# Performance work log

Measured on AMD Instinct MI355X. Metric: run time of the kernel, lower is better.

Reference implementation:

```python
import jax, jax.numpy as jnp
import numpy as np

HEADS = 8
DIM_HEAD = 64          # dim // 8
INNER = HEADS * DIM_HEAD
LANDMARKS = 256        # dim // 2
PINV_ITERS = 6
KER = 33               # residual_conv_kernel
DIM = 512


def layer_norm(x, gamma, beta, eps=1e-5):
    mu = x.mean(-1, keepdims=True)
    var = x.var(-1, keepdims=True)
    return (x - mu) / jnp.sqrt(var + eps) * gamma + beta


def moore_penrose_pinv(x, iters):
    # x: [b, h, m, m]; Newton-Schulz iteration, init z = x^T / (max colsum * max rowsum)
    abs_x = jnp.abs(x)
    col = abs_x.sum(-1)
    row = abs_x.sum(-2)
    z = jnp.swapaxes(x, -1, -2) / (jnp.max(col) * jnp.max(row))
    I = jnp.eye(x.shape[-1], dtype=x.dtype)
    for _ in range(iters):
        xz = x @ z
        z = 0.25 * z @ (13.0 * I - xz @ (15.0 * I - xz @ (7.0 * I - xz)))
    return z


def nystrom_attention(x, w_qkv, w_out, b_out, conv_w):
    b, n, _ = x.shape
    qkv = x @ w_qkv                                   # [b, n, 3*inner]
    q, k, v = jnp.split(qkv, 3, axis=-1)
    split = lambda t: t.reshape(b, n, HEADS, DIM_HEAD).transpose(0, 2, 1, 3)  # [b,h,n,dh]
    q, k, v = split(q), split(k), split(v)
    q = q * (DIM_HEAD ** -0.5)

    l = n // LANDMARKS  # n chosen divisible by num_landmarks (no padding branch)
    q_land = q.reshape(b, HEADS, LANDMARKS, l, DIM_HEAD).mean(3)  # [b,h,m,dh]
    k_land = k.reshape(b, HEADS, LANDMARKS, l, DIM_HEAD).mean(3)

    sim1 = jnp.einsum('bhid,bhjd->bhij', q, k_land)       # [b,h,n,m]
    sim2 = jnp.einsum('bhid,bhjd->bhij', q_land, k_land)  # [b,h,m,m]
    sim3 = jnp.einsum('bhid,bhjd->bhij', q_land, k)       # [b,h,m,n]
    attn1 = jax.nn.softmax(sim1, -1)
    attn2 = jax.nn.softmax(sim2, -1)
    attn3 = jax.nn.softmax(sim3, -1)

    attn2_inv = moore_penrose_pinv(attn2, PINV_ITERS)
    out = (attn1 @ attn2_inv) @ (attn3 @ v)               # [b,h,n,dh]

    # depthwise residual conv over sequence dim: Conv2d(h, h, (33,1), groups=h, no bias)
    res = jax.lax.conv_general_dilated(
        v, conv_w, window_strides=(1, 1),
        padding=((KER // 2, KER // 2), (0, 0)),
        dimension_numbers=('NCHW', 'OIHW', 'NCHW'),
        feature_group_count=HEADS)
    out = out + res

    out = out.transpose(0, 2, 1, 3).reshape(b, n, INNER)
    return out @ w_out + b_out  # dropout is identity at eval


def setup_inputs() -> dict:
    key = jax.random.key(0)
    ks = jax.random.split(key, 7)
    b, n = 4, 8192
    return {
        'x': jax.random.normal(ks[0], (b, n, DIM), dtype=jnp.float32),
        'gamma': jnp.ones((DIM,), jnp.float32),
        'beta': jnp.zeros((DIM,), jnp.float32),
        'w_qkv': jax.random.normal(ks[1], (DIM, 3 * INNER), jnp.float32) * 0.02,
        'w_out': jax.random.normal(ks[2], (INNER, DIM), jnp.float32) * 0.02,
        'b_out': jnp.zeros((DIM,), jnp.float32),
        'conv_w': jax.random.normal(ks[3], (HEADS, 1, KER, 1), jnp.float32) * 0.02,
    }


def reference(x, gamma, beta, w_qkv, w_out, b_out, conv_w):
    return x + nystrom_attention(layer_norm(x, gamma, beta), w_qkv, w_out, b_out, conv_w)
```

## Files before the change

### kernel.cpp

```cpp
#include <hip/hip_runtime.h>
#include <hip/hip_bf16.h>
#include <utility>


typedef unsigned short ushort_t;
typedef __attribute__((ext_vector_type(8))) short short8;
typedef __attribute__((ext_vector_type(4))) float f32x4;
typedef __attribute__((ext_vector_type(16))) float f32x16;

#define GPTR(p) ((const __attribute__((address_space(1))) void*)(p))
#define LPTR(p) ((__attribute__((address_space(3))) void*)(p))

__device__ inline float bf2f(ushort_t u) {
  union { unsigned int i; float f; } x; x.i = ((unsigned int)u) << 16; return x.f;
}
__device__ inline ushort_t f2bf(float f) {
  union { float f; unsigned int i; } x; x.f = f;
  unsigned int r = x.i + 0x7FFF + ((x.i >> 16) & 1);
  return (ushort_t)(r >> 16);
}

__global__ __launch_bounds__(256) void ln_bf16(const float* __restrict__ x,
                                               const float* __restrict__ g,
                                               const float* __restrict__ be,
                                               ushort_t* __restrict__ out) {
  int row = blockIdx.x; int t = threadIdx.x;
  const float* xr = x + (size_t)row * 512;
  float2 v = *(const float2*)(xr + 2 * t);
  float s = v.x + v.y, qs = v.x * v.x + v.y * v.y;
#pragma unroll
  for (int o = 32; o > 0; o >>= 1) { s += __shfl_xor(s, o); qs += __shfl_xor(qs, o); }
  __shared__ float ps[4], pq[4];
  if ((t & 63) == 0) { ps[t >> 6] = s; pq[t >> 6] = qs; }
  __syncthreads();
  s = ps[0] + ps[1] + ps[2] + ps[3];
  qs = pq[0] + pq[1] + pq[2] + pq[3];
  float mu = s * (1.f / 512.f);
  float var = qs * (1.f / 512.f) - mu * mu;
  float rstd = rsqrtf(var + 1e-5f);
  float o0 = (v.x - mu) * rstd * g[2 * t] + be[2 * t];
  float o1 = (v.y - mu) * rstd * g[2 * t + 1] + be[2 * t + 1];
  unsigned int pk = (unsigned int)f2bf(o0) | ((unsigned int)f2bf(o1) << 16);
  *(unsigned int*)(out + (size_t)row * 512 + 2 * t) = pk;
}

__global__ __launch_bounds__(256) void wtrans(const float* __restrict__ in,
                                              ushort_t* __restrict__ outw,
                                              int K, int N) {
  __shared__ float tile[64][65];
  int kb = blockIdx.x * 64, nb = blockIdx.y * 64, t = threadIdx.x;
  for (int i = t; i < 4096; i += 256) {
    int r = i >> 6, c = i & 63;
    tile[r][c] = in[(size_t)(kb + r) * N + nb + c];
  }
  __syncthreads();
  for (int i = t; i < 4096; i += 256) {
    int r = i >> 6, c = i & 63;
    outw[(size_t)(nb + r) * K + kb + c] = f2bf(tile[c][r]);
  }
}

__global__ __launch_bounds__(256) void gemm_qkv_mfma(const short* __restrict__ Abf,
                                                     const short* __restrict__ Wt,
                                                     ushort_t* __restrict__ q,
                                                     ushort_t* __restrict__ k,
                                                     ushort_t* __restrict__ vT) {
  int bm0 = blockIdx.x * 128, bn0 = blockIdx.y * 128;
  __shared__ __align__(16) short As[128 * 32];
  __shared__ __align__(16) short Bs[128 * 32];
  int t = threadIdx.x, l = t & 63, w = t >> 6;
  int wr = w >> 1, wc = w & 1;
  int arow = w * 32 + (l >> 2);
  int akoff = (l & 3) * 8;
  const short* ag = Abf + (size_t)(bm0 + arow) * 512 + akoff;
  const short* bg = Wt + (size_t)(bn0 + arow) * 512 + akoff;
  short* Adst = As + w * 1024;
  short* Bdst = Bs + w * 1024;
  int lr = l & 15, lk = (l >> 4) * 8;
  const short* Ard = As + (wr * 64 + lr) * 32 + lk;
  const short* Brd = Bs + (wc * 64 + lr) * 32 + lk;
  f32x4 acc[16];
#pragma unroll
  for (int i = 0; i < 16; i++) acc[i] = (f32x4){0.f, 0.f, 0.f, 0.f};
  for (int k0 = 0; k0 < 512; k0 += 32) {
    __builtin_amdgcn_global_load_lds(GPTR(ag + k0), LPTR(Adst), 16, 0, 0);
    __builtin_amdgcn_global_load_lds(GPTR(ag + k0 + 16 * 512), LPTR(Adst + 512), 16, 0, 0);
    __builtin_amdgcn_global_load_lds(GPTR(bg + k0), LPTR(Bdst), 16, 0, 0);
    __builtin_amdgcn_global_load_lds(GPTR(bg + k0 + 16 * 512), LPTR(Bdst + 512), 16, 0, 0);
    __syncthreads();
    short8 af[4], bf[4];
#pragma unroll
    for (int mf = 0; mf < 4; mf++) af[mf] = *(const short8*)(Ard + mf * 512);
#pragma unroll
    for (int nf = 0; nf < 4; nf++) bf[nf] = *(const short8*)(Brd + nf * 512);
#pragma unroll
    for (int mf = 0; mf < 4; mf++)
#pragma unroll
      for (int nf = 0; nf < 4; nf++)
        acc[mf * 4 + nf] = __builtin_amdgcn_mfma_f32_16x16x32_bf16(af[mf], bf[nf], acc[mf * 4 + nf], 0, 0, 0);
    __syncthreads();
  }
#pragma unroll
  for (int mf = 0; mf < 4; mf++)
#pragma unroll
    for (int nf = 0; nf < 4; nf++) {
      int gn = bn0 + wc * 64 + nf * 16 + (l & 15);
      int part = gn >> 9, head = (gn >> 6) & 7, d = gn & 63;
      int rbase = bm0 + wr * 64 + mf * 16 + ((l >> 4) << 2);
      int bhead = (rbase >> 13) * 8 + head;
      if (part == 2) {
        union { ushort_t s[4]; unsigned long long u; } p4;
#pragma unroll
        for (int i = 0; i < 4; i++) p4.s[i] = f2bf(acc[mf * 4 + nf][i]);
        *(unsigned long long*)(vT + ((size_t)bhead * 64 + d) * 8192 + (rbase & 8191)) = p4.u;
      } else {
#pragma unroll
        for (int i = 0; i < 4; i++) {
          int gm = rbase + i;
          size_t dst = ((size_t)bhead * 8192 + (gm & 8191)) * 64 + d;
          float val = acc[mf * 4 + nf][i];
          if (part == 0) q[dst] = f2bf(val * 0.125f);
          else k[dst] = f2bf(val);
        }
      }
    }
}

__global__ __launch_bounds__(256) void gemm_out_mfma(const ushort_t* __restrict__ outh,
                                                     const short* __restrict__ Wt,
                                                     const float* __restrict__ x,
                                                     const float* __restrict__ bo,
                                                     float* __restrict__ out) {
  int bn0 = blockIdx.x * 128, bm0 = blockIdx.y * 128;
  __shared__ __align__(16) short As[128 * 32];
  __shared__ __align__(16) short Bs[128 * 32];
  int t = threadIdx.x, l = t & 63, w = t >> 6;
  int wr = w >> 1, wc = w & 1;
  int arow = w * 32 + (l >> 2);
  int akoff = (l & 3) * 8;
  int gm0 = bm0 + arow, gm1 = gm0 + 16;
  const short* bg = Wt + (size_t)(bn0 + arow) * 512 + akoff;
  short* Adst = As + w * 1024;
  short* Bdst = Bs + w * 1024;
  int lr = l & 15, lk = (l >> 4) * 8;
  const short* Ard = As + (wr * 64 + lr) * 32 + lk;
  const short* Brd = Bs + (wc * 64 + lr) * 32 + lk;
  f32x4 acc[16];
#pragma unroll
  for (int i = 0; i < 16; i++) acc[i] = (f32x4){0.f, 0.f, 0.f, 0.f};
  for (int k0 = 0; k0 < 512; k0 += 32) {
    int kk = k0 + akoff;
    const ushort_t* a0 = outh + ((size_t)((gm0 >> 13) * 8 + (kk >> 6)) * 8192 + (gm0 & 8191)) * 64 + (kk & 63);
    const ushort_t* a1 = outh + ((size_t)((gm1 >> 13) * 8 + (kk >> 6)) * 8192 + (gm1 & 8191)) * 64 + (kk & 63);
    __builtin_amdgcn_global_load_lds(GPTR(a0), LPTR(Adst), 16, 0, 0);
    __builtin_amdgcn_global_load_lds(GPTR(a1), LPTR(Adst + 512), 16, 0, 0);
    __builtin_amdgcn_global_load_lds(GPTR(bg + k0), LPTR(Bdst), 16, 0, 0);
    __builtin_amdgcn_global_load_lds(GPTR(bg + k0 + 16 * 512), LPTR(Bdst + 512), 16, 0, 0);
    __syncthreads();
    short8 af[4], bf[4];
#pragma unroll
    for (int mf = 0; mf < 4; mf++) af[mf] = *(const short8*)(Ard + mf * 512);
#pragma unroll
    for (int nf = 0; nf < 4; nf++) bf[nf] = *(const short8*)(Brd + nf * 512);
#pragma unroll
    for (int mf = 0; mf < 4; mf++)
#pragma unroll
      for (int nf = 0; nf < 4; nf++)
        acc[mf * 4 + nf] = __builtin_amdgcn_mfma_f32_16x16x32_bf16(af[mf], bf[nf], acc[mf * 4 + nf], 0, 0, 0);
    __syncthreads();
  }
#pragma unroll
  for (int mf = 0; mf < 4; mf++)
#pragma unroll
    for (int nf = 0; nf < 4; nf++) {
      int gn = bn0 + wc * 64 + nf * 16 + (l & 15);
      int rbase = bm0 + wr * 64 + mf * 16 + ((l >> 4) << 2);
#pragma unroll
      for (int i = 0; i < 4; i++) {
        int gm = rbase + i;
        size_t o = (size_t)gm * 512 + gn;
        out[o] = x[o] + bo[gn] + acc[mf * 4 + nf][i];
      }
    }
}

__global__ void land_kernel(const ushort_t* __restrict__ q, const ushort_t* __restrict__ k,
                            float* __restrict__ qlf, float* __restrict__ klf,
                            ushort_t* __restrict__ qlh, ushort_t* __restrict__ klh) {
  int bh = blockIdx.y, mi = blockIdx.x, d = threadIdx.x;
  size_t base = ((size_t)bh * 8192 + (size_t)mi * 32) * 64 + d;
  float sq = 0.f, sk = 0.f;
  for (int j = 0; j < 32; j++) {
    sq += bf2f(q[base + (size_t)j * 64]);
    sk += bf2f(k[base + (size_t)j * 64]);
  }
  size_t o = ((size_t)bh * 256 + mi) * 64 + d;
  float aq = sq * (1.f / 32.f), ak = sk * (1.f / 32.f);
  qlf[o] = aq; klf[o] = ak;
  qlh[o] = f2bf(aq); klh[o] = f2bf(ak);
}

__global__ __launch_bounds__(256) void sim2_kernel(const float* __restrict__ ql,
                                                   const float* __restrict__ kl,
                                                   ushort_t* __restrict__ xh,
                                                   ushort_t* __restrict__ xl) {
  int bh = blockIdx.y, row = blockIdx.x, t = threadIdx.x;
  __shared__ float qrow[64];
  __shared__ float red[256];
  if (t < 64) qrow[t] = ql[((size_t)bh * 256 + row) * 64 + t];
  __syncthreads();
  const float* kr = kl + ((size_t)bh * 256 + t) * 64;
  float s = 0.f;
#pragma unroll
  for (int kd = 0; kd < 64; kd++) s = fmaf(qrow[kd], kr[kd], s);
  red[t] = s; __syncthreads();
  for (int off = 128; off > 0; off >>= 1) { if (t < off) red[t] = fmaxf(red[t], red[t + off]); __syncthreads(); }
  float mx = red[0]; __syncthreads();
  float pv = __expf(s - mx);
  red[t] = pv; __syncthreads();
  for (int off = 128; off > 0; off >>= 1) { if (t < off) red[t] += red[t + off]; __syncthreads(); }
  float pn = pv / red[0];
  size_t idx = ((size_t)bh << 16) + (size_t)row * 256 + t;
  ushort_t hi = f2bf(pn);
  xh[idx] = hi;
  xl[idx] = f2bf(pn - bf2f(hi));
}

__global__ __launch_bounds__(256) void abssum_kernel(const ushort_t* __restrict__ xh,
                                                     const ushort_t* __restrict__ xl,
                                                     float* __restrict__ rowsum,
                                                     float* __restrict__ colsum) {
  int bh = blockIdx.x, t = threadIdx.x;
  size_t off = (size_t)bh << 16;
  float s = 0.f;
  for (int c = 0; c < 256; c++) {
    size_t i = off + (size_t)t * 256 + c;
    s += fabsf(bf2f(xh[i]) + bf2f(xl[i]));
  }
  rowsum[bh * 256 + t] = s;
  float s2 = 0.f;
  for (int r = 0; r < 256; r++) {
    size_t i = off + (size_t)r * 256 + t;
    s2 += fabsf(bf2f(xh[i]) + bf2f(xl[i]));
  }
  colsum[bh * 256 + t] = s2;
}

__global__ __launch_bounds__(256) void pinv_scale_kernel(const float* __restrict__ rowsum,
                                                         const float* __restrict__ colsum,
                                                         float* __restrict__ scl) {
  int t = threadIdx.x;
  float m1 = 0.f, m2 = 0.f;
  for (int i = t; i < 8192; i += 256) { m1 = fmaxf(m1, rowsum[i]); m2 = fmaxf(m2, colsum[i]); }
  __shared__ float r1[256], r2[256];
  r1[t] = m1; r2[t] = m2; __syncthreads();
  for (int off = 128; off > 0; off >>= 1) {
    if (t < off) { r1[t] = fmaxf(r1[t], r1[t + off]); r2[t] = fmaxf(r2[t], r2[t + off]); }
    __syncthreads();
  }
  if (t == 0) scl[0] = 1.f / (r1[0] * r2[0]);
}

__global__ __launch_bounds__(256) void zinit_kernel(const ushort_t* __restrict__ xh,
                                                    const ushort_t* __restrict__ xl,
                                                    const float* __restrict__ scl,
                                                    ushort_t* __restrict__ zrh,
                                                    ushort_t* __restrict__ zrl,
                                                    ushort_t* __restrict__ zth,
                                                    ushort_t* __restrict__ ztl) {
  int bh = blockIdx.y, i = blockIdx.x, j = threadIdx.x;
  size_t off = (size_t)bh << 16;
  float s = scl[0];
  size_t src1 = off + (size_t)j * 256 + i;
  float v1 = (bf2f(xh[src1]) + bf2f(xl[src1])) * s;
  size_t dst = off + (size_t)i * 256 + j;
  ushort_t h1 = f2bf(v1);
  zrh[dst] = h1; zrl[dst] = f2bf(v1 - bf2f(h1));
  size_t src2 = off + (size_t)i * 256 + j;
  float v2 = (bf2f(xh[src2]) + bf2f(xl[src2])) * s;
  ushort_t h2 = f2bf(v2);
  zth[dst] = h2; ztl[dst] = f2bf(v2 - bf2f(h2));
}

template<int MODE, int FULL, int WRLO>
__global__ __launch_bounds__(256) void bmm_ns(
    const ushort_t* __restrict__ Agh, const ushort_t* __restrict__ Agl,
    const ushort_t* __restrict__ Bgh, const ushort_t* __restrict__ Bgl,
    const ushort_t* __restrict__ Exh, const ushort_t* __restrict__ Exl,
    ushort_t* __restrict__ C1h, ushort_t* __restrict__ C1l,
    ushort_t* __restrict__ C2h, ushort_t* __restrict__ C2l) {
  __shared__ __align__(16) char smem[FULL ? 65536 : 32768];
  char* AhB = smem;
  char* BhB = smem + 16384;
  char* AlB = smem + 32768;
  char* BlB = smem + 49152;

  int t = threadIdx.x, l = t & 63, w = t >> 6, h = l >> 5;
  int tile = blockIdx.x, bh = blockIdx.y;
  int tr = (tile >> 2) << 6, tc = (tile & 3) << 6;
  size_t off = (size_t)bh << 16;

  int id0 = w * 64 + l, id1 = id0 + 256;
  int r0 = id0 >> 3, cs0 = (id0 & 7) ^ (r0 & 7);
  int r1 = id1 >> 3, cs1 = (id1 & 7) ^ (r1 & 7);

  auto stage = [&](int s, int d) {
    int k0 = s << 6;
    int db = d * 8192;
    __builtin_amdgcn_global_load_lds(GPTR(Agh + off + (size_t)(tr + r0) * 256 + k0 + cs0 * 8), LPTR(AhB + db + w * 1024), 16, 0, 0);
    __builtin_amdgcn_global_load_lds(GPTR(Agh + off + (size_t)(tr + r1) * 256 + k0 + cs1 * 8), LPTR(AhB + db + w * 1024 + 4096), 16, 0, 0);
    __builtin_amdgcn_global_load_lds(GPTR(Bgh + off + (size_t)(tc + r0) * 256 + k0 + cs0 * 8), LPTR(BhB + db + w * 1024), 16, 0, 0);
    __builtin_amdgcn_global_load_lds(GPTR(Bgh + off + (size_t)(tc + r1) * 256 + k0 + cs1 * 8), LPTR(BhB + db + w * 1024 + 4096), 16, 0, 0);
    if (FULL) {
      __builtin_amdgcn_global_load_lds(GPTR(Agl + off + (size_t)(tr + r0) * 256 + k0 + cs0 * 8), LPTR(AlB + db + w * 1024), 16, 0, 0);
      __builtin_amdgcn_global_load_lds(GPTR(Agl + off + (size_t)(tr + r1) * 256 + k0 + cs1 * 8), LPTR(AlB + db + w * 1024 + 4096), 16, 0, 0);
      __builtin_amdgcn_global_load_lds(GPTR(Bgl + off + (size_t)(tc + r0) * 256 + k0 + cs0 * 8), LPTR(BlB + db + w * 1024), 16, 0, 0);
      __builtin_amdgcn_global_load_lds(GPTR(Bgl + off + (size_t)(tc + r1) * 256 + k0 + cs1 * 8), LPTR(BlB + db + w * 1024 + 4096), 16, 0, 0);
    }
  };

  f32x16 acc;
#pragma unroll
  for (int i = 0; i < 16; i++) acc[i] = 0.f;

  int rA = ((w >> 1) << 5) + (l & 31);
  int rB = ((w & 1) << 5) + (l & 31);
  int baA = rA << 7, baB = rB << 7;

  stage(0, 0);
  __syncthreads();
  for (int s = 0; s < 4; s++) {
    if (s < 3) stage(s + 1, (s + 1) & 1);
    int db = (s & 1) * 8192;
#pragma unroll
    for (int kk = 0; kk < 4; kk++) {
      int swA = (((kk << 1) + h) ^ (rA & 7)) << 4;
      int swB = (((kk << 1) + h) ^ (rB & 7)) << 4;
      short8 afh = *(const short8*)(AhB + db + baA + swA);
      short8 bfh = *(const short8*)(BhB + db + baB + swB);
      acc = __builtin_amdgcn_mfma_f32_32x32x16_bf16(afh, bfh, acc, 0, 0, 0);
      if (FULL) {
        short8 afl = *(const short8*)(AlB + db + baA + swA);
        short8 bfl = *(const short8*)(BlB + db + baB + swB);
        acc = __builtin_amdgcn_mfma_f32_32x32x16_bf16(afh, bfl, acc, 0, 0, 0);
        acc = __builtin_amdgcn_mfma_f32_32x32x16_bf16(afl, bfh, acc, 0, 0, 0);
      }
    }
    __syncthreads();
  }

  int qr = tr + ((w >> 1) << 5);
  int nloc = ((w & 1) << 5) + (l & 31);
  int gn = tc + nloc;
  ushort_t his[16], los[16];
  int ms[16];
#pragma unroll
  for (int reg = 0; reg < 16; reg++) {
    int m = (reg & 3) + ((reg >> 2) << 3) + (h << 2);
    int gm = qr + m;
    float e = acc[reg];
    if (MODE == 1) {
      size_t ei = off + (size_t)gm * 256 + gn;
      float ex = bf2f(Exh[ei]);
      if (FULL) ex += bf2f(Exl[ei]);
      e = e - 7.f * ex + (gm == gn ? 15.f : 0.f);
    } else if (MODE == 2) {
      e = (gm == gn ? 13.f : 0.f) - e;
    } else if (MODE == 3) {
      e *= 0.25f;
    }
    his[reg] = f2bf(e);
    if (WRLO) los[reg] = f2bf(e - bf2f(his[reg]));
    ms[reg] = ((w >> 1) << 5) + m;
  }
  ushort_t* Whi = (ushort_t*)smem;
  ushort_t* Wlo = ((ushort_t*)smem) + 4608;
#pragma unroll
  for (int reg = 0; reg < 16; reg++) {
    Whi[nloc * 72 + ms[reg]] = his[reg];
    if (WRLO) Wlo[nloc * 72 + ms[reg]] = los[reg];
  }
  __syncthreads();
  {
    int rr = t >> 2, seg = (t & 3) << 4;
    uint4 h0 = *(const uint4*)(Whi + rr * 72 + seg);
    uint4 h1 = *(const uint4*)(Whi + rr * 72 + seg + 8);
    size_t d2 = off + (size_t)(tc + rr) * 256 + tr + seg;
    *(uint4*)(C2h + d2) = h0; *(uint4*)(C2h + d2 + 8) = h1;
    if (WRLO) {
      uint4 l0 = *(const uint4*)(Wlo + rr * 72 + seg);
      uint4 l1 = *(const uint4*)(Wlo + rr * 72 + seg + 8);
      *(uint4*)(C2l + d2) = l0; *(uint4*)(C2l + d2 + 8) = l1;
    }
  }
  if (MODE == 0 || MODE == 3) {
    __syncthreads();
#pragma unroll
    for (int reg = 0; reg < 16; reg++) {
      Whi[ms[reg] * 72 + nloc] = his[reg];
      if (WRLO) Wlo[ms[reg] * 72 + nloc] = los[reg];
    }
    __syncthreads();
    int rr = t >> 2, seg = (t & 3) << 4;
    uint4 h0 = *(const uint4*)(Whi + rr * 72 + seg);
    uint4 h1 = *(const uint4*)(Whi + rr * 72 + seg + 8);
    size_t d1 = off + (size_t)(tr + rr) * 256 + tc + seg;
    *(uint4*)(C1h + d1) = h0; *(uint4*)(C1h + d1 + 8) = h1;
    if (WRLO) {
      uint4 l0 = *(const uint4*)(Wlo + rr * 72 + seg);
      uint4 l1 = *(const uint4*)(Wlo + rr * 72 + seg + 8);
      *(uint4*)(C1l + d1) = l0; *(uint4*)(C1l + d1 + 8) = l1;
    }
  }
}

__global__ __launch_bounds__(256) void flash_mfma(
    const ushort_t* __restrict__ qsrc, const ushort_t* __restrict__ ksrc,
    const ushort_t* __restrict__ vts, ushort_t* __restrict__ outb,
    float* __restrict__ pOT, float* __restrict__ pM, float* __restrict__ pL,
    const ushort_t* __restrict__ convsrc, const float* __restrict__ wcv,
    int nq, int nkv, int vt_stride, int nsplit, int write_partial) {
  __shared__ __align__(16) char smem[38400];
  ushort_t* Ks = (ushort_t*)smem;
  ushort_t* Vs = (ushort_t*)(smem + 8192);

  int t = threadIdx.x, l = t & 63, w = t >> 6, h = l >> 5, ql = l & 31;
  int qtile = blockIdx.x, sp = blockIdx.y, bh = blockIdx.z;
  int chunk = nkv / nsplit;
  int kvbase = sp * chunk;
  int qg = qtile * 128 + w * 32 + ql;

  const ushort_t* qp = qsrc + ((size_t)bh * nq + qg) * 64;
  short8 qf[4];
#pragma unroll
  for (int kk = 0; kk < 4; kk++) qf[kk] = *(const short8*)(qp + kk * 16 + h * 8);

  f32x16 acc0, acc1;
#pragma unroll
  for (int i = 0; i < 16; i++) { acc0[i] = 0.f; acc1[i] = 0.f; }

  int c0 = w * 64 + l, c1 = c0 + 256;
  int r0 = c0 >> 3, s0 = ((c0 & 7) ^ (r0 & 7)) << 3;
  int r1 = c1 >> 3, s1 = ((c1 & 7) ^ (r1 & 7)) << 3;
  const ushort_t* kb = ksrc + (size_t)bh * nkv * 64;
  const ushort_t* vb = vts + (size_t)bh * 64 * vt_stride;

  float mrun = -1e30f, lrun = 0.f;
  int ntiles = chunk >> 6;
  for (int it = 0; it < ntiles; it++) {
    int kvt = kvbase + it * 64;
    __syncthreads();
    __builtin_amdgcn_global_load_lds(GPTR(kb + (size_t)(kvt + r0) * 64 + s0), LPTR(Ks + w * 512), 16, 0, 0);
    __builtin_amdgcn_global_load_lds(GPTR(kb + (size_t)(kvt + r1) * 64 + s1), LPTR(Ks + 2048 + w * 512), 16, 0, 0);
    __builtin_amdgcn_global_load_lds(GPTR(vb + (size_t)r0 * vt_stride + kvt + s0), LPTR(Vs + w * 512), 16, 0, 0);
    __builtin_amdgcn_global_load_lds(GPTR(vb + (size_t)r1 * vt_stride + kvt + s1), LPTR(Vs + 2048 + w * 512), 16, 0, 0);
    __syncthreads();

    f32x16 st0, st1;
#pragma unroll
    for (int i = 0; i < 16; i++) { st0[i] = 0.f; st1[i] = 0.f; }
#pragma unroll
    for (int kk = 0; kk < 4; kk++) {
      int ch = kk * 2 + h;
      short8 kf0 = *(const short8*)(Ks + ql * 64 + ((ch ^ (ql & 7)) << 3));
      short8 kf1 = *(const short8*)(Ks + (32 + ql) * 64 + ((ch ^ (ql & 7)) << 3));
      st0 = __builtin_amdgcn_mfma_f32_32x32x16_bf16(kf0, qf[kk], st0, 0, 0, 0);
      st1 = __builtin_amdgcn_mfma_f32_32x32x16_bf16(kf1, qf[kk], st1, 0, 0, 0);
    }

    float tm = -1e30f;
#pragma unroll
    for (int r2 = 0; r2 < 16; r2++) { tm = fmaxf(tm, st0[r2]); tm = fmaxf(tm, st1[r2]); }
    tm = fmaxf(tm, __shfl_xor(tm, 32));
    float mnew = fmaxf(mrun, tm);
    float scal = __expf(mrun - mnew);
    float tsum = 0.f;
#pragma unroll
    for (int r2 = 0; r2 < 16; r2++) {
      float p0 = __expf(st0[r2] - mnew); st0[r2] = p0; tsum += p0;
      float p1 = __expf(st1[r2] - mnew); st1[r2] = p1; tsum += p1;
    }
    tsum += __shfl_xor(tsum, 32);
    lrun = lrun * scal + tsum;
    mrun = mnew;
#pragma unroll
    for (int r2 = 0; r2 < 16; r2++) { acc0[r2] *= scal; acc1[r2] *= scal; }

#pragma unroll
    for (int nf = 0; nf < 2; nf++) {
      f32x16 stv = (nf == 0) ? st0 : st1;
      unsigned int pk[8], sw[8];
#pragma unroll
      for (int g2 = 0; g2 < 4; g2++) {
        pk[g2 * 2]     = (unsigned int)f2bf(stv[g2 * 4])     | ((unsigned int)f2bf(stv[g2 * 4 + 1]) << 16);
        pk[g2 * 2 + 1] = (unsigned int)f2bf(stv[g2 * 4 + 2]) | ((unsigned int)f2bf(stv[g2 * 4 + 3]) << 16);
      }
#pragma unroll
      for (int i2 = 0; i2 < 8; i2++) sw[i2] = (unsigned int)__shfl_xor((int)pk[i2], 32);
      union { unsigned int u[4]; short8 s; } bfr0, bfr1;
      if (h == 0) {
        bfr0.u[0] = pk[0]; bfr0.u[1] = pk[1]; bfr0.u[2] = sw[0]; bfr0.u[3] = sw[1];
        bfr1.u[0] = pk[4]; bfr1.u[1] = pk[5]; bfr1.u[2] = sw[4]; bfr1.u[3] = sw[5];
      } else {
        bfr0.u[0] = sw[2]; bfr0.u[1] = sw[3]; bfr0.u[2] = pk[2]; bfr0.u[3] = pk[3];
        bfr1.u[0] = sw[6]; bfr1.u[1] = sw[7]; bfr1.u[2] = pk[6]; bfr1.u[3] = pk[7];
      }
#pragma unroll
      for (int ks2 = 0; ks2 < 2; ks2++) {
        int ch2 = nf * 4 + ks2 * 2 + h;
        short8 vf0 = *(const short8*)(Vs + ql * 64 + ((ch2 ^ (ql & 7)) << 3));
        short8 vf1 = *(const short8*)(Vs + (32 + ql) * 64 + ((ch2 ^ (ql & 7)) << 3));
        short8 pf = ks2 ? bfr1.s : bfr0.s;
        acc0 = __builtin_amdgcn_mfma_f32_32x32x16_bf16(vf0, pf, acc0, 0, 0, 0);
        acc1 = __builtin_amdgcn_mfma_f32_32x32x16_bf16(vf1, pf, acc1, 0, 0, 0);
      }
    }
  }

  if (write_partial) {
    size_t ob = (size_t)bh * nsplit + sp;
#pragma unroll
    for (int r2 = 0; r2 < 16; r2++) {
      int row = (r2 & 3) + 8 * (r2 >> 2) + 4 * h;
      pOT[(ob * 64 + row) * nq + qg] = acc0[r2];
      pOT[(ob * 64 + 32 + row) * nq + qg] = acc1[r2];
    }
    if (h == 0) { pM[ob * nq + qg] = mrun; pL[ob * nq + qg] = lrun; }
  } else {
    float inv = 1.f / lrun;
    __syncthreads();
    ushort_t* Otb = (ushort_t*)smem;
    ushort_t* vsb = (ushort_t*)(smem + 17408);
#pragma unroll
    for (int r2 = 0; r2 < 16; r2++) {
      int row = (r2 & 3) + 8 * (r2 >> 2) + 4 * h;
      Otb[row * 136 + w * 32 + ql] = f2bf(acc0[r2] * inv);
      Otb[(32 + row) * 136 + w * 32 + ql] = f2bf(acc1[r2] * inv);
    }
    {
      int r = t >> 2, part = t & 3;
      const ushort_t* src = convsrc + ((size_t)bh * 64 + r) * 8192;
      int n0 = qtile * 128;
#pragma unroll
      for (int j = 0; j < 5; j++) {
        int col = part * 40 + j * 8;
        int gn = n0 - 16 + col;
        if (gn >= 0 && gn + 7 < 8192) {
          *(uint2*)&vsb[r * 164 + col] = *(const uint2*)(src + gn);
          *(uint2*)&vsb[r * 164 + col + 4] = *(const uint2*)(src + gn + 4);
        } else {
#pragma unroll
          for (int e = 0; e < 8; e++) {
            int g2 = gn + e;
            vsb[r * 164 + col + e] = (g2 >= 0 && g2 < 8192) ? src[g2] : (ushort_t)0;
          }
        }
      }
    }
    __syncthreads();
    int d = t & 63, ng = t >> 6;
    float win[64];
#pragma unroll
    for (int j2 = 0; j2 < 16; j2++) {
      uint2 u = *(const uint2*)&vsb[d * 164 + ng * 32 + j2 * 4];
      const ushort_t* us = (const ushort_t*)&u;
      win[j2 * 4 + 0] = bf2f(us[0]); win[j2 * 4 + 1] = bf2f(us[1]);
      win[j2 * 4 + 2] = bf2f(us[2]); win[j2 * 4 + 3] = bf2f(us[3]);
    }
    int hh = bh & 7;
    float o[32];
#pragma unroll
    for (int i = 0; i < 32; i++) o[i] = 0.f;
#pragma unroll
    for (int kk = 0; kk < 33; kk++) {
      float wv = wcv[hh * 33 + kk];
#pragma unroll
      for (int i = 0; i < 32; i++) o[i] = fmaf(wv, win[i + kk], o[i]);
    }
    ushort_t* op = outb + ((size_t)bh * nq + qtile * 128 + ng * 32) * 64 + d;
#pragma unroll
    for (int i = 0; i < 32; i++) {
      float attn = bf2f(Otb[d * 136 + ng * 32 + i]);
      op[(size_t)i * 64] = f2bf(attn + o[i]);
    }
  }
}

#define NSPLIT 8
__global__ __launch_bounds__(256) void flash_combine(const float* __restrict__ pOT,
                                                     const float* __restrict__ pM,
                                                     const float* __restrict__ pL,
                                                     ushort_t* __restrict__ T, int nq) {
  int bh = blockIdx.x, qq = threadIdx.x;
  float ms[NSPLIT], ww[NSPLIT];
  float M = -1e30f;
#pragma unroll
  for (int s = 0; s < NSPLIT; s++) {
    ms[s] = pM[((size_t)bh * NSPLIT + s) * nq + qq];
    M = fmaxf(M, ms[s]);
  }
  float L = 0.f;
#pragma unroll
  for (int s = 0; s < NSPLIT; s++) {
    ww[s] = __expf(ms[s] - M);
    L += ww[s] * pL[((size_t)bh * NSPLIT + s) * nq + qq];
  }
  float invL = 1.f / L;
  ushort_t* tp = T + ((size_t)bh * nq + qq) * 64;
  for (int d0 = 0; d0 < 64; d0 += 8) {
    union { ushort_t s[8]; uint4 u; } o8;
#pragma unroll
    for (int j = 0; j < 8; j++) {
      int d = d0 + j;
      float o = 0.f;
#pragma unroll
      for (int s = 0; s < NSPLIT; s++)
        o += ww[s] * pOT[(((size_t)bh * NSPLIT + s) * 64 + d) * nq + qq];
      o8.s[j] = f2bf(o * invL);
    }
    *(uint4*)(tp + d0) = o8.u;
  }
}

__global__ __launch_bounds__(256) void zu_kernel(const ushort_t* __restrict__ zh,
                                                 const ushort_t* __restrict__ zl,
                                                 const ushort_t* __restrict__ T,
                                                 ushort_t* __restrict__ UT) {
  __shared__ __align__(16) ushort_t Ts[16384];
  __shared__ __align__(16) ushort_t Ub[64 * 40];
  int bh = blockIdx.y, r0 = blockIdx.x * 32, t = threadIdx.x;
  {
    const uint4* src = (const uint4*)(T + ((size_t)bh << 14));
    uint4* dst = (uint4*)Ts;
    for (int i = t; i < 2048; i += 256) dst[i] = src[i];
  }
  __syncthreads();
  int rloc = t >> 3, dseg = (t & 7) << 3;
  size_t zoff = ((size_t)bh << 16) + (size_t)(r0 + rloc) * 256;
  float acc[8];
#pragma unroll
  for (int j = 0; j < 8; j++) acc[j] = 0.f;
  for (int c0 = 0; c0 < 256; c0 += 8) {
    uint4 zhv = *(const uint4*)(zh + zoff + c0);
    uint4 zlv = *(const uint4*)(zl + zoff + c0);
    const ushort_t* z8h = (const ushort_t*)&zhv;
    const ushort_t* z8l = (const ushort_t*)&zlv;
#pragma unroll
    for (int cc = 0; cc < 8; cc++) {
      float zv = bf2f(z8h[cc]) + bf2f(z8l[cc]);
      short8 tv = *(const short8*)(Ts + (c0 + cc) * 64 + dseg);
#pragma unroll
      for (int j = 0; j < 8; j++) acc[j] = fmaf(zv, bf2f((ushort_t)tv[j]), acc[j]);
    }
  }
#pragma unroll
  for (int j = 0; j < 8; j++) Ub[(dseg + j) * 40 + rloc] = f2bf(acc[j]);
  __syncthreads();
  int d = t >> 2, rseg = (t & 3) << 3;
  uint4 v = *(const uint4*)(Ub + d * 40 + rseg);
  *(uint4*)(UT + ((size_t)bh * 64 + d) * 256 + r0 + rseg) = v;
}

extern "C" void kernel_launch(void* const* d_in, const int* in_sizes, int n_in,
                              void* d_out, int out_size, void* d_ws, size_t ws_size,
                              hipStream_t stream) {
  (void)in_sizes; (void)n_in; (void)out_size; (void)ws_size;
  const float* x     = (const float*)d_in[0];
  const float* g     = (const float*)d_in[1];
  const float* be    = (const float*)d_in[2];
  const float* wqkv  = (const float*)d_in[3];
  const float* wout  = (const float*)d_in[4];
  const float* bout  = (const float*)d_in[5];
  const float* convw = (const float*)d_in[6];
  float* out = (float*)d_out;

  char* base = (char*)d_ws;
  size_t off = 0;
  auto alloc = [&](size_t bytes) -> void* {
    void* r = base + off; off = (off + bytes + 255) & ~(size_t)255; return r;
  };
  const size_t NBH = (size_t)32 * 8192 * 64;
  const size_t M2 = (size_t)32 * 256 * 256 * 2;
  ushort_t* q     = (ushort_t*)alloc(NBH * 2);
  ushort_t* k     = (ushort_t*)alloc(NBH * 2);
  ushort_t* vT    = (ushort_t*)alloc(NBH * 2);
  ushort_t* outh  = (ushort_t*)alloc(NBH * 2);
  float*    qlf   = (float*)alloc((size_t)32 * 256 * 64 * 4);
  float*    klf   = (float*)alloc((size_t)32 * 256 * 64 * 4);
  ushort_t* qlh   = (ushort_t*)alloc((size_t)32 * 256 * 64 * 2);
  ushort_t* klh   = (ushort_t*)alloc((size_t)32 * 256 * 64 * 2);
  ushort_t* xh    = (ushort_t*)alloc(M2);
  ushort_t* xl    = (ushort_t*)alloc(M2);
  ushort_t* zArh  = (ushort_t*)alloc(M2);
  ushort_t* zArl  = (ushort_t*)alloc(M2);
  ushort_t* zAth  = (ushort_t*)alloc(M2);
  ushort_t* zAtl  = (ushort_t*)alloc(M2);
  ushort_t* zBrh  = (ushort_t*)alloc(M2);
  ushort_t* zBrl  = (ushort_t*)alloc(M2);
  ushort_t* zBth  = (ushort_t*)alloc(M2);
  ushort_t* zBtl  = (ushort_t*)alloc(M2);
  ushort_t* ARh   = (ushort_t*)alloc(M2);
  ushort_t* ARl   = (ushort_t*)alloc(M2);
  ushort_t* ATh   = (ushort_t*)alloc(M2);
  ushort_t* ATl   = (ushort_t*)alloc(M2);
  ushort_t* DTh   = (ushort_t*)alloc(M2);
  ushort_t* DTl   = (ushort_t*)alloc(M2);
  ushort_t* FTh   = (ushort_t*)alloc(M2);
  ushort_t* FTl   = (ushort_t*)alloc(M2);
  float*    rowsum = (float*)alloc(8192 * 4);
  float*    colsum = (float*)alloc(8192 * 4);
  float*    scl   = (float*)alloc(64);
  ushort_t* T     = (ushort_t*)alloc((size_t)32 * 256 * 64 * 2);
  ushort_t* UT    = (ushort_t*)alloc((size_t)32 * 64 * 256 * 2);
  ushort_t* Wqkvt = (ushort_t*)alloc((size_t)1536 * 512 * 2);
  ushort_t* Woutt = (ushort_t*)alloc((size_t)512 * 512 * 2);
  short* Abf = (short*)xh;
  float* pOT = (float*)ARh;
  float* pM  = (float*)DTh;
  float* pL  = (float*)DTh + 65536;

  ln_bf16<<<32768, 256, 0, stream>>>(x, g, be, (ushort_t*)Abf);
  wtrans<<<dim3(8, 24), 256, 0, stream>>>(wqkv, Wqkvt, 512, 1536);
  wtrans<<<dim3(8, 8), 256, 0, stream>>>(wout, Woutt, 512, 512);
  gemm_qkv_mfma<<<dim3(256, 12), 256, 0, stream>>>(Abf, (const short*)Wqkvt, q, k, vT);
  land_kernel<<<dim3(256, 32), 64, 0, stream>>>(q, k, qlf, klf, qlh, klh);
  sim2_kernel<<<dim3(256, 32), 256, 0, stream>>>(qlf, klf, xh, xl);
  abssum_kernel<<<32, 256, 0, stream>>>(xh, xl, rowsum, colsum);
  pinv_scale_kernel<<<1, 256, 0, stream>>>(rowsum, colsum, scl);
  zinit_kernel<<<dim3(256, 32), 256, 0, stream>>>(xh, xl, scl, zArh, zArl, zAth, zAtl);

  ushort_t *zrh = zArh, *zrl = zArl, *zth = zAth, *ztl = zAtl;
  ushort_t *nrh = zBrh, *nrl = zBrl, *nth = zBth, *ntl = zBtl;
  dim3 nsgrid(16, 32);
  for (int it = 0; it < 6; it++) {
    if (it < 5) {
      bmm_ns<0, 0, 0><<<nsgrid, 256, 0, stream>>>(xh, xl, zth, ztl, xh, xl, ARh, ARl, ATh, ATl);
      bmm_ns<1, 0, 0><<<nsgrid, 256, 0, stream>>>(ARh, ARl, ATh, ATl, ARh, ARl, DTh, DTl, DTh, DTl);
      bmm_ns<2, 0, 0><<<nsgrid, 256, 0, stream>>>(ARh, ARl, DTh, DTl, xh, xl, FTh, FTl, FTh, FTl);
      if (it == 4)
        bmm_ns<3, 0, 1><<<nsgrid, 256, 0, stream>>>(zrh, zrl, FTh, FTl, xh, xl, nrh, nrl, nth, ntl);
      else
        bmm_ns<3, 0, 0><<<nsgrid, 256, 0, stream>>>(zrh, zrl, FTh, FTl, xh, xl, nrh, nrl, nth, ntl);
    } else {
      bmm_ns<0, 1, 1><<<nsgrid, 256, 0, stream>>>(xh, xl, zth, ztl, xh, xl, ARh, ARl, ATh, ATl);
      bmm_ns<1, 1, 1><<<nsgrid, 256, 0, stream>>>(ARh, ARl, ATh, ATl, ARh, ARl, DTh, DTl, DTh, DTl);
      bmm_ns<2, 1, 1><<<nsgrid, 256, 0, stream>>>(ARh, ARl, DTh, DTl, xh, xl, FTh, FTl, FTh, FTl);
      bmm_ns<3, 1, 1><<<nsgrid, 256, 0, stream>>>(zrh, zrl, FTh, FTl, xh, xl, nrh, nrl, nth, ntl);
    }
    std::swap(zrh, nrh); std::swap(zrl, nrl);
    std::swap(zth, nth); std::swap(ztl, ntl);
  }

  flash_mfma<<<dim3(2, 8, 32), 256, 0, stream>>>(qlh, k, vT, T, pOT, pM, pL,
                                                 vT, convw, 256, 8192, 8192, 8, 1);
  flash_combine<<<32, 256, 0, stream>>>(pOT, pM, pL, T, 256);
  zu_kernel<<<dim3(8, 32), 256, 0, stream>>>(zrh, zrl, T, UT);
  flash_mfma<<<dim3(64, 1, 32), 256, 0, stream>>>(q, klh, UT, outh, pOT, pM, pL,
                                                  vT, convw, 8192, 256, 256, 1, 0);
  gemm_out_mfma<<<dim3(4, 256), 256, 0, stream>>>(outh, (const short*)Woutt, x, bout, out);
}
```

Before: 678.8 us.

## Double-buffer LDS in QKV/out GEMMs and vectorize landmark mean kernel

Both projection GEMMs now use two LDS buffers, so the global-to-LDS load for the next K slice is issued before the MFMAs on the current slice. The aim is to hide global load latency behind compute, at the cost of doubling the LDS footprint per block (32KB) and possibly lowering occupancy. The landmark kernel is rewritten so each wave handles one landmark, using 16-byte vector loads and a cross-lane shuffle reduction. This replaces 64-thread blocks doing strided scalar loads. The remaining loop body is not shown, so whether a barrier is kept after the MFMAs to protect the buffer being refilled cannot be confirmed.

```diff
diff --git a/kernel.cpp b/kernel.cpp
--- a/kernel.cpp
+++ b/kernel.cpp
@@ -66,28 +66,35 @@
                                                      ushort_t* __restrict__ k,
                                                      ushort_t* __restrict__ vT) {
   int bm0 = blockIdx.x * 128, bn0 = blockIdx.y * 128;
-  __shared__ __align__(16) short As[128 * 32];
-  __shared__ __align__(16) short Bs[128 * 32];
+  __shared__ __align__(16) short As[2 * 4096];
+  __shared__ __align__(16) short Bs[2 * 4096];
   int t = threadIdx.x, l = t & 63, w = t >> 6;
   int wr = w >> 1, wc = w & 1;
   int arow = w * 32 + (l >> 2);
   int akoff = (l & 3) * 8;
   const short* ag = Abf + (size_t)(bm0 + arow) * 512 + akoff;
   const short* bg = Wt + (size_t)(bn0 + arow) * 512 + akoff;
-  short* Adst = As + w * 1024;
-  short* Bdst = Bs + w * 1024;
   int lr = l & 15, lk = (l >> 4) * 8;
-  const short* Ard = As + (wr * 64 + lr) * 32 + lk;
-  const short* Brd = Bs + (wc * 64 + lr) * 32 + lk;
-  f32x4 acc[16];
-#pragma unroll
-  for (int i = 0; i < 16; i++) acc[i] = (f32x4){0.f, 0.f, 0.f, 0.f};
-  for (int k0 = 0; k0 < 512; k0 += 32) {
+
+  auto stage = [&](int k0, int d) {
+    short* Adst = As + d * 4096 + w * 1024;
+    short* Bdst = Bs + d * 4096 + w * 1024;
     __builtin_amdgcn_global_load_lds(GPTR(ag + k0), LPTR(Adst), 16, 0, 0);
     __builtin_amdgcn_global_load_lds(GPTR(ag + k0 + 16 * 512), LPTR(Adst + 512), 16, 0, 0);
     __builtin_amdgcn_global_load_lds(GPTR(bg + k0), LPTR(Bdst), 16, 0, 0);
     __builtin_amdgcn_global_load_lds(GPTR(bg + k0 + 16 * 512), LPTR(Bdst + 512), 16, 0, 0);
-    __syncthreads();
+  };
+
+  f32x4 acc[16];
+#pragma unroll
+  for (int i = 0; i < 16; i++) acc[i] = (f32x4){0.f, 0.f, 0.f, 0.f};
+
+  stage(0, 0);
+  __syncthreads();
+  for (int s = 0; s < 16; s++) {
+    if (s < 15) stage((s + 1) * 32, (s + 1) & 1);
+    const short* Ard = As + (s & 1) * 4096 + (wr * 64 + lr) * 32 + lk;
+    const short* Brd = Bs + (s & 1) * 4096 + (wc * 64 + lr) * 32 + lk;
     short8 af[4], bf[4];
 #pragma unroll
     for (int mf = 0; mf < 4; mf++) af[mf] = *(const short8*)(Ard + mf * 512);
@@ -132,31 +139,38 @@
                                                      const float* __restrict__ bo,
                                                      float* __restrict__ out) {
   int bn0 = blockIdx.x * 128, bm0 = blockIdx.y * 128;
-  __shared__ __align__(16) short As[128 * 32];
-  __shared__ __align__(16) short Bs[128 * 32];
+  __shared__ __align__(16) short As[2 * 4096];
+  __shared__ __align__(16) short Bs[2 * 4096];
   int t = threadIdx.x, l = t & 63, w = t >> 6;
   int wr = w >> 1, wc = w & 1;
   int arow = w * 32 + (l >> 2);
   int akoff = (l & 3) * 8;
   int gm0 = bm0 + arow, gm1 = gm0 + 16;
   const short* bg = Wt + (size_t)(bn0 + arow) * 512 + akoff;
-  short* Adst = As + w * 1024;
-  short* Bdst = Bs + w * 1024;
   int lr = l & 15, lk = (l >> 4) * 8;
-  const short* Ard = As + (wr * 64 + lr) * 32 + lk;
-  const short* Brd = Bs + (wc * 64 + lr) * 32 + lk;
-  f32x4 acc[16];
-#pragma unroll
-  for (int i = 0; i < 16; i++) acc[i] = (f32x4){0.f, 0.f, 0.f, 0.f};
-  for (int k0 = 0; k0 < 512; k0 += 32) {
+
+  auto stage = [&](int k0, int d) {
     int kk = k0 + akoff;
     const ushort_t* a0 = outh + ((size_t)((gm0 >> 13) * 8 + (kk >> 6)) * 8192 + (gm0 & 8191)) * 64 + (kk & 63);
     const ushort_t* a1 = outh + ((size_t)((gm1 >> 13) * 8 + (kk >> 6)) * 8192 + (gm1 & 8191)) * 64 + (kk & 63);
+    short* Adst = As + d * 4096 + w * 1024;
+    short* Bdst = Bs + d * 4096 + w * 1024;
     __builtin_amdgcn_global_load_lds(GPTR(a0), LPTR(Adst), 16, 0, 0);
     __builtin_amdgcn_global_load_lds(GPTR(a1), LPTR(Adst + 512), 16, 0, 0);
     __builtin_amdgcn_global_load_lds(GPTR(bg + k0), LPTR(Bdst), 16, 0, 0);
     __builtin_amdgcn_global_load_lds(GPTR(bg + k0 + 16 * 512), LPTR(Bdst + 512), 16, 0, 0);
-    __syncthreads();
+  };
+
+  f32x4 acc[16];
+#pragma unroll
+  for (int i = 0; i < 16; i++) acc[i] = (f32x4){0.f, 0.f, 0.f, 0.f};
+
+  stage(0, 0);
+  __syncthreads();
+  for (int s = 0; s < 16; s++) {
+    if (s < 15) stage((s + 1) * 32, (s + 1) & 1);
+    const short* Ard = As + (s & 1) * 4096 + (wr * 64 + lr) * 32 + lk;
+    const short* Brd = Bs + (s & 1) * 4096 + (wc * 64 + lr) * 32 + lk;
     short8 af[4], bf[4];
 #pragma unroll
     for (int mf = 0; mf < 4; mf++) af[mf] = *(const short8*)(Ard + mf * 512);
@@ -184,20 +198,44 @@
     }
 }
 
-__global__ void land_kernel(const ushort_t* __restrict__ q, const ushort_t* __restrict__ k,
-                            float* __restrict__ qlf, float* __restrict__ klf,
-                            ushort_t* __restrict__ qlh, ushort_t* __restrict__ klh) {
-  int bh = blockIdx.y, mi = blockIdx.x, d = threadIdx.x;
-  size_t base = ((size_t)bh * 8192 + (size_t)mi * 32) * 64 + d;
-  float sq = 0.f, sk = 0.f;
-  for (int j = 0; j < 32; j++) {
-    sq += bf2f(q[base + (size_t)j * 64]);
-    sk += bf2f(k[base + (size_t)j * 64]);
-  }
-  size_t o = ((size_t)bh * 256 + mi) * 64 + d;
-  float aq = sq * (1.f / 32.f), ak = sk * (1.f / 32.f);
-  qlf[o] = aq; klf[o] = ak;
-  qlh[o] = f2bf(aq); klh[o] = f2bf(ak);
+__global__ __launch_bounds__(256) void land_kernel(const ushort_t* __restrict__ q,
+                                                   const ushort_t* __restrict__ k,
+                                                   float* __restrict__ qlf,
+                                                   float* __restrict__ klf,
+                                                   ushort_t* __restrict__ qlh,
+                                                   ushort_t* __restrict__ klh) {
+  int bh = blockIdx.y;
+  int wv = threadIdx.x >> 6, l = threadIdx.x & 63;
+  int mi = blockIdx.x * 4 + wv;
+  size_t base = ((size_t)bh * 8192 + (size_t)mi * 32) * 64;
+  float sq[8], sk[8];
+#pragma unroll
+  for (int e = 0; e < 8; e++) { sq[e] = 0.f; sk[e] = 0.f; }
+#pragma unroll
+  for (int j = 0; j < 4; j++) {
+    uint4 uq = *(const uint4*)(q + base + (size_t)(j * 64 + l) * 8);
+    uint4 uk = *(const uint4*)(k + base + (size_t)(j * 64 + l) * 8);
+    const ushort_t* aq = (const ushort_t*)&uq;
+    const ushort_t* ak = (const ushort_t*)&uk;
+#pragma unroll
+    for (int e = 0; e < 8; e++) { sq[e] += bf2f(aq[e]); sk[e] += bf2f(ak[e]); }
+  }
+#pragma unroll
+  for (int m = 8; m < 64; m <<= 1)
+#pragma unroll
+    for (int e = 0; e < 8; e++) { sq[e] += __shfl_xor(sq[e], m); sk[e] += __shfl_xor(sk[e], m); }
+  if (l < 8) {
+    size_t o = ((size_t)bh * 256 + mi) * 64 + l * 8;
+    union { ushort_t s[8]; uint4 u; } hq, hk;
+#pragma unroll
+    for (int e = 0; e < 8; e++) {
+      float aq2 = sq[e] * (1.f / 32.f), ak2 = sk[e] * (1.f / 32.f);
+      qlf[o + e] = aq2; klf[o + e] = ak2;
+      hq.s[e] = f2bf(aq2); hk.s[e] = f2bf(ak2);
+    }
+    *(uint4*)(qlh + o) = hq.u;
+    *(uint4*)(klh + o) = hk.u;
+  }
 }
 
 __global__ __launch_bounds__(256) void sim2_kernel(const float* __restrict__ ql,
@@ -723,7 +761,7 @@
   wtrans<<<dim3(8, 24), 256, 0, stream>>>(wqkv, Wqkvt, 512, 1536);
   wtrans<<<dim3(8, 8), 256, 0, stream>>>(wout, Woutt, 512, 512);
   gemm_qkv_mfma<<<dim3(256, 12), 256, 0, stream>>>(Abf, (const short*)Wqkvt, q, k, vT);
-  land_kernel<<<dim3(256, 32), 64, 0, stream>>>(q, k, qlf, klf, qlh, klh);
+  land_kernel<<<dim3(64, 32), 256, 0, stream>>>(q, k, qlf, klf, qlh, klh);
   sim2_kernel<<<dim3(256, 32), 256, 0, stream>>>(qlf, klf, xh, xl);
   abssum_kernel<<<32, 256, 0, stream>>>(xh, xl, rowsum, colsum);
   pinv_scale_kernel<<<1, 256, 0, stream>>>(rowsum, colsum, scl);
```

After: 713.5 us. 5.1% more time.
